# Optimization experiments

Measured on AMD Instinct MI355X. Metric: run time of the kernel, lower is better.

Reference implementation:

```python
import jax, jax.numpy as jnp
import numpy as np

MARGIN = 0.3
EPS = 1e-12


def setup_inputs() -> dict:
    key = jax.random.key(0)
    k1, k2 = jax.random.split(key)
    n, d = 4096, 1024
    inputs = jax.random.normal(k1, (n, d), dtype=jnp.float32)
    targets = jax.random.randint(k2, (n,), 0, 64, dtype=jnp.int64)
    return {"inputs": inputs, "targets": targets}


def reference(inputs, targets):
    n = inputs.shape[0]
    # pairwise Euclidean distance matrix: ||xi||^2 + ||xj||^2 - 2 xi.xj
    sq = jnp.sum(inputs * inputs, axis=1)  # [n]
    dist2 = sq[:, None] + sq[None, :] - 2.0 * (inputs @ inputs.T)
    dist = jnp.sqrt(jnp.clip(dist2, EPS))  # [n, n]
    # same-label mask (includes diagonal, matching original)
    mask = targets[:, None] == targets[None, :]
    # fused masked row-wise hard mining
    neg_inf = jnp.asarray(-jnp.inf, dist.dtype)
    pos_inf = jnp.asarray(jnp.inf, dist.dtype)
    dist_ap = jnp.max(jnp.where(mask, dist, neg_inf), axis=1)  # hardest positive
    dist_an = jnp.min(jnp.where(mask, pos_inf, dist), axis=1)  # hardest negative
    # MarginRankingLoss with y=1: mean(relu(margin - (dist_an - dist_ap)))
    loss = jnp.mean(jnp.maximum(MARGIN - (dist_an - dist_ap), 0.0))
    prec = jnp.sum((dist_an > dist_ap).astype(jnp.float32)) / n
    return (loss, prec)
```

## Files before the change

kernel.cpp:

```cpp
#include <hip/hip_runtime.h>
#include <stdint.h>

#define MARGIN 0.3f
#define EPS 1e-12f

typedef __attribute__((ext_vector_type(8))) __bf16 bf16x8;
typedef __attribute__((ext_vector_type(4))) float f32x4;

__device__ __forceinline__ unsigned short f2bf(float f) {
    unsigned u = __float_as_uint(f);
    unsigned r = (u + 0x7FFFu + ((u >> 16) & 1u)) >> 16;
    return (unsigned short)r;
}

#define GLD16(gp, lp)                                                     \
    __builtin_amdgcn_global_load_lds(                                     \
        (const __attribute__((address_space(1))) void*)(gp),              \
        (__attribute__((address_space(3))) void*)(lp), 16, 0, 0)

__global__ __launch_bounds__(256) void prep_kernel(
    const float* __restrict__ X, unsigned short* __restrict__ Xbf,
    float* __restrict__ sqg, unsigned* __restrict__ apb,
    unsigned* __restrict__ anb, int d) {
    const int row = blockIdx.x;
    const int tid = threadIdx.x;
    const float4* Xr = (const float4*)(X + (size_t)row * d);
    float s = 0.0f;
    for (int idx = tid; idx < (d >> 2); idx += blockDim.x) {
        float4 v = Xr[idx];
        s += v.x * v.x + v.y * v.y + v.z * v.z + v.w * v.w;
        ushort4 o;
        o.x = f2bf(v.x); o.y = f2bf(v.y); o.z = f2bf(v.z); o.w = f2bf(v.w);
        ((ushort4*)(Xbf + (size_t)row * d))[idx] = o;
    }
    __shared__ float red[4];
    for (int off = 32; off > 0; off >>= 1) s += __shfl_down(s, off, 64);
    const int wave = tid >> 6, lane = tid & 63;
    if (lane == 0) red[wave] = s;
    __syncthreads();
    if (tid == 0) {
        sqg[row] = red[0] + red[1] + red[2] + red[3];
        apb[row] = 0u;
        anb[row] = 0x7F800000u;
    }
}

#define BM 128
#define BN 128
#define BK 32

__global__ __launch_bounds__(256) void tri_gemm(
    const unsigned short* __restrict__ Xbf, const float* __restrict__ sqg,
    const int* __restrict__ tgt, unsigned* __restrict__ apb,
    unsigned* __restrict__ anb, int n, int d) {
    __shared__ unsigned short ldsA[BM * BK];
    __shared__ unsigned short ldsB[BN * BK];

    const int tid  = threadIdx.x;
    const int lane = tid & 63;
    const int wave = tid >> 6;
    const int wm = wave >> 1, wn = wave & 1;
    const int lo = lane & 15, hi = lane >> 4;
    const int rowBase = blockIdx.y * BM;
    const int colBase = blockIdx.x * BN;

    const int lrow = lane >> 2;
    const int lk   = (lane & 3) * 8;

    f32x4 acc[4][4] = {};

    for (int k0 = 0; k0 < d; k0 += BK) {
#pragma unroll
        for (int c2 = 0; c2 < 2; ++c2) {
            const int c = wave * 2 + c2;
            const unsigned short* gA =
                Xbf + (size_t)(rowBase + c * 16 + lrow) * d + k0 + lk;
            GLD16(gA, &ldsA[c * 512]);
            const unsigned short* gB =
                Xbf + (size_t)(colBase + c * 16 + lrow) * d + k0 + lk;
            GLD16(gB, &ldsB[c * 512]);
        }
        asm volatile("s_waitcnt vmcnt(0)" ::: "memory");
        __syncthreads();

        bf16x8 a[4], b[4];
#pragma unroll
        for (int mi = 0; mi < 4; ++mi)
            a[mi] = *(const bf16x8*)&ldsA[(wm * 64 + mi * 16 + lo) * BK + hi * 8];
#pragma unroll
        for (int ni = 0; ni < 4; ++ni)
            b[ni] = *(const bf16x8*)&ldsB[(wn * 64 + ni * 16 + lo) * BK + hi * 8];
#pragma unroll
        for (int mi = 0; mi < 4; ++mi)
#pragma unroll
            for (int ni = 0; ni < 4; ++ni)
                acc[mi][ni] = __builtin_amdgcn_mfma_f32_16x16x32_bf16(
                    a[mi], b[ni], acc[mi][ni], 0, 0, 0);
        __syncthreads();
    }

    float sqj[4];
    int   tj[4];
#pragma unroll
    for (int ni = 0; ni < 4; ++ni) {
        const int gj = colBase + wn * 64 + ni * 16 + lo;
        sqj[ni] = sqg[gj];
        tj[ni]  = tgt[gj];
    }
#pragma unroll
    for (int mi = 0; mi < 4; ++mi) {
#pragma unroll
        for (int j = 0; j < 4; ++j) {
            const int gi = rowBase + wm * 64 + mi * 16 + hi * 4 + j;
            const float sqi = sqg[gi];
            const int   ti  = tgt[gi];
            float ap = 0.0f;
            float an = __uint_as_float(0x7F800000u);
#pragma unroll
            for (int ni = 0; ni < 4; ++ni) {
                const float d2 = sqi + sqj[ni] - 2.0f * acc[mi][ni][j];
                const float dist = sqrtf(fmaxf(d2, EPS));
                if (ti == tj[ni]) ap = fmaxf(ap, dist);
                else              an = fminf(an, dist);
            }
#pragma unroll
            for (int m = 1; m < 16; m <<= 1) {
                ap = fmaxf(ap, __shfl_xor(ap, m, 64));
                an = fminf(an, __shfl_xor(an, m, 64));
            }
            if (lo == 0) {
                atomicMax(&apb[gi], __float_as_uint(ap));
                atomicMin(&anb[gi], __float_as_uint(an));
            }
        }
    }
}

__global__ __launch_bounds__(256) void finalize_kernel(
    const unsigned* __restrict__ apb, const unsigned* __restrict__ anb,
    float* __restrict__ out, int n) {
    const int tid = threadIdx.x;
    float ls = 0.0f, pc = 0.0f;
    for (int i = tid; i < n; i += blockDim.x) {
        const float ap = __uint_as_float(apb[i]);
        const float an = __uint_as_float(anb[i]);
        ls += fmaxf(MARGIN - (an - ap), 0.0f);
        pc += (an > ap) ? 1.0f : 0.0f;
    }
    __shared__ float rl[4], rp[4];
    for (int off = 32; off > 0; off >>= 1) {
        ls += __shfl_down(ls, off, 64);
        pc += __shfl_down(pc, off, 64);
    }
    const int wave = tid >> 6, lane = tid & 63;
    if (lane == 0) { rl[wave] = ls; rp[wave] = pc; }
    __syncthreads();
    if (tid == 0) {
        out[0] = (rl[0] + rl[1] + rl[2] + rl[3]) / (float)n;
        out[1] = (rp[0] + rp[1] + rp[2] + rp[3]) / (float)n;
    }
}

__global__ __launch_bounds__(256) void fb_zero(float* __restrict__ out) {
    if (threadIdx.x == 0) { out[0] = 0.0f; out[1] = 0.0f; }
}

__global__ __launch_bounds__(256) void fb_row(
    const float* __restrict__ X, const int* __restrict__ tgt,
    float* __restrict__ out, int n, int d) {
    __shared__ float xi[4096];
    const int i = blockIdx.x;
    const int tid = threadIdx.x;
    for (int k = tid; k < d; k += 256) xi[k] = X[(size_t)i * d + k];
    __syncthreads();
    const int ti = tgt[i];
    float ap = 0.0f;
    float an = __uint_as_float(0x7F800000u);
    for (int j = tid; j < n; j += 256) {
        const float4* Xj = (const float4*)(X + (size_t)j * d);
        float s = 0.0f;
        for (int k4 = 0; k4 < (d >> 2); ++k4) {
            float4 v = Xj[k4];
            float4 u = *(const float4*)&xi[k4 * 4];
            float dx = u.x - v.x, dy = u.y - v.y, dz = u.z - v.z, dw = u.w - v.w;
            s += dx * dx + dy * dy + dz * dz + dw * dw;
        }
        const float dist = sqrtf(fmaxf(s, EPS));
        if (tgt[j] == ti) ap = fmaxf(ap, dist);
        else              an = fminf(an, dist);
    }
    for (int m = 1; m < 64; m <<= 1) {
        ap = fmaxf(ap, __shfl_xor(ap, m, 64));
        an = fminf(an, __shfl_xor(an, m, 64));
    }
    __shared__ float rap[4], ran[4];
    const int wave = tid >> 6, lane = tid & 63;
    if (lane == 0) { rap[wave] = ap; ran[wave] = an; }
    __syncthreads();
    if (tid == 0) {
        ap = fmaxf(fmaxf(rap[0], rap[1]), fmaxf(rap[2], rap[3]));
        an = fminf(fminf(ran[0], ran[1]), fminf(ran[2], ran[3]));
        atomicAdd(&out[0], fmaxf(MARGIN - (an - ap), 0.0f));
        atomicAdd(&out[1], (an > ap) ? 1.0f : 0.0f);
    }
}

__global__ __launch_bounds__(64) void fb_scale(float* __restrict__ out, float inv_n) {
    if (threadIdx.x == 0) { out[0] *= inv_n; out[1] *= inv_n; }
}

extern "C" void kernel_launch(void* const* d_in, const int* in_sizes, int n_in,
                              void* d_out, int out_size, void* d_ws, size_t ws_size,
                              hipStream_t stream) {
    const float* X   = (const float*)d_in[0];
    const int*   tgt = (const int*)d_in[1];
    const int n = in_sizes[1];
    const int d = in_sizes[0] / n;

    const size_t need = (size_t)n * d * 2 + (size_t)n * 4 * 3;
    if (ws_size >= need) {
        char* ws = (char*)d_ws;
        unsigned short* Xbf = (unsigned short*)ws;
        float*    sqg = (float*)(ws + (size_t)n * d * 2);
        unsigned* apb = (unsigned*)((char*)sqg + (size_t)n * 4);
        unsigned* anb = apb + n;

        prep_kernel<<<n, 256, 0, stream>>>(X, Xbf, sqg, apb, anb, d);
        dim3 grid(n / BN, n / BM);
        tri_gemm<<<grid, 256, 0, stream>>>(Xbf, sqg, tgt, apb, anb, n, d);
        finalize_kernel<<<1, 256, 0, stream>>>(apb, anb, (float*)d_out, n);
    } else {
        fb_zero<<<1, 256, 0, stream>>>((float*)d_out);
        fb_row<<<n, 256, 0, stream>>>(X, tgt, (float*)d_out, n, d);
        fb_scale<<<1, 64, 0, stream>>>((float*)d_out, 1.0f / (float)n);
    }
}
```

Measured before the change: 145.8 us.

## Exploit distance symmetry with triangular tiles, double-buffer LDS, fuse finalize

Launches only lower-triangular 128x128 tiles of the symmetric distance matrix. Each off-diagonal tile also reduces along columns and updates the column rows' hardest positive and negative with atomics, which roughly halves the GEMM work. The K loop now double-buffers LDS so the next tile's global loads overlap the MFMAs. The separate finalize kernel is folded into the last finishing block through an atomic counter. The cost is extra column-reduction shuffles and atomics, plus a global-counter barrier pattern.

```diff
diff --git a/kernel.cpp b/kernel.cpp
--- a/kernel.cpp
+++ b/kernel.cpp
@@ -21,7 +21,7 @@
 __global__ __launch_bounds__(256) void prep_kernel(
     const float* __restrict__ X, unsigned short* __restrict__ Xbf,
     float* __restrict__ sqg, unsigned* __restrict__ apb,
-    unsigned* __restrict__ anb, int d) {
+    unsigned* __restrict__ anb, unsigned* __restrict__ ctr, int d) {
     const int row = blockIdx.x;
     const int tid = threadIdx.x;
     const float4* Xr = (const float4*)(X + (size_t)row * d);
@@ -42,6 +42,7 @@
         sqg[row] = red[0] + red[1] + red[2] + red[3];
         apb[row] = 0u;
         anb[row] = 0x7F800000u;
+        if (row == 0) ctr[0] = 0u;
     }
 }
 
@@ -52,51 +53,72 @@
 __global__ __launch_bounds__(256) void tri_gemm(
     const unsigned short* __restrict__ Xbf, const float* __restrict__ sqg,
     const int* __restrict__ tgt, unsigned* __restrict__ apb,
-    unsigned* __restrict__ anb, int n, int d) {
-    __shared__ unsigned short ldsA[BM * BK];
-    __shared__ unsigned short ldsB[BN * BK];
+    unsigned* __restrict__ anb, unsigned* __restrict__ ctr,
+    float* __restrict__ out, int n, int d, int nblk) {
+    __shared__ unsigned short ldsA[2][BM * BK];
+    __shared__ unsigned short ldsB[2][BN * BK];
 
     const int tid  = threadIdx.x;
     const int lane = tid & 63;
     const int wave = tid >> 6;
     const int wm = wave >> 1, wn = wave & 1;
     const int lo = lane & 15, hi = lane >> 4;
-    const int rowBase = blockIdx.y * BM;
-    const int colBase = blockIdx.x * BN;
+
+    const int bid = blockIdx.x;
+    int bi = (int)((sqrtf(8.0f * (float)bid + 1.0f) - 1.0f) * 0.5f);
+    while ((bi + 1) * (bi + 2) / 2 <= bid) ++bi;
+    while (bi * (bi + 1) / 2 > bid) --bi;
+    const int bj = bid - bi * (bi + 1) / 2;
+    const int rowBase = bi * BM;
+    const int colBase = bj * BN;
+    const bool offdiag = (bi != bj);
 
     const int lrow = lane >> 2;
     const int lk   = (lane & 3) * 8;
 
     f32x4 acc[4][4] = {};
 
-    for (int k0 = 0; k0 < d; k0 += BK) {
-#pragma unroll
-        for (int c2 = 0; c2 < 2; ++c2) {
-            const int c = wave * 2 + c2;
-            const unsigned short* gA =
-                Xbf + (size_t)(rowBase + c * 16 + lrow) * d + k0 + lk;
-            GLD16(gA, &ldsA[c * 512]);
-            const unsigned short* gB =
-                Xbf + (size_t)(colBase + c * 16 + lrow) * d + k0 + lk;
-            GLD16(gB, &ldsB[c * 512]);
-        }
-        asm volatile("s_waitcnt vmcnt(0)" ::: "memory");
-        __syncthreads();
-
+    const int nt = d / BK;
+    int cur = 0;
+#pragma unroll
+    for (int c2 = 0; c2 < 2; ++c2) {
+        const int c = wave * 2 + c2;
+        GLD16(Xbf + (size_t)(rowBase + c * 16 + lrow) * d + lk, &ldsA[0][c * 512]);
+        GLD16(Xbf + (size_t)(colBase + c * 16 + lrow) * d + lk, &ldsB[0][c * 512]);
+    }
+    asm volatile("s_waitcnt vmcnt(0)" ::: "memory");
+    __syncthreads();
+
+    for (int t = 0; t < nt; ++t) {
+        if (t + 1 < nt) {
+            const int k0 = (t + 1) * BK;
+#pragma unroll
+            for (int c2 = 0; c2 < 2; ++c2) {
+                const int c = wave * 2 + c2;
+                GLD16(Xbf + (size_t)(rowBase + c * 16 + lrow) * d + k0 + lk,
+                      &ldsA[cur ^ 1][c * 512]);
+                GLD16(Xbf + (size_t)(colBase + c * 16 + lrow) * d + k0 + lk,
+                      &ldsB[cur ^ 1][c * 512]);
+            }
+        }
         bf16x8 a[4], b[4];
 #pragma unroll
         for (int mi = 0; mi < 4; ++mi)
-            a[mi] = *(const bf16x8*)&ldsA[(wm * 64 + mi * 16 + lo) * BK + hi * 8];
+            a[mi] = *(const bf16x8*)&ldsA[cur][(wm * 64 + mi * 16 + lo) * BK + hi * 8];
 #pragma unroll
         for (int ni = 0; ni < 4; ++ni)
-            b[ni] = *(const bf16x8*)&ldsB[(wn * 64 + ni * 16 + lo) * BK + hi * 8];
+            b[ni] = *(const bf16x8*)&ldsB[cur][(wn * 64 + ni * 16 + lo) * BK + hi * 8];
 #pragma unroll
         for (int mi = 0; mi < 4; ++mi)
 #pragma unroll
             for (int ni = 0; ni < 4; ++ni)
                 acc[mi][ni] = __builtin_amdgcn_mfma_f32_16x16x32_bf16(
                     a[mi], b[ni], acc[mi][ni], 0, 0, 0);
-        __syncthreads();
+        if (t + 1 < nt) {
+            asm volatile("s_waitcnt vmcnt(0)" ::: "memory");
+            __syncthreads();
+            cur ^= 1;
+        }
     }
 
     float sqj[4];
@@ -107,6 +129,10 @@
         sqj[ni] = sqg[gj];
         tj[ni]  = tgt[gj];
     }
+    float cap[4], can[4];
+#pragma unroll
+    for (int ni = 0; ni < 4; ++ni) { cap[ni] = 0.0f; can[ni] = __uint_as_float(0x7F800000u); }
+
 #pragma unroll
     for (int mi = 0; mi < 4; ++mi) {
 #pragma unroll
@@ -120,8 +146,13 @@
             for (int ni = 0; ni < 4; ++ni) {
                 const float d2 = sqi + sqj[ni] - 2.0f * acc[mi][ni][j];
                 const float dist = sqrtf(fmaxf(d2, EPS));
-                if (ti == tj[ni]) ap = fmaxf(ap, dist);
-                else              an = fminf(an, dist);
+                if (ti == tj[ni]) {
+                    ap = fmaxf(ap, dist);
+                    cap[ni] = fmaxf(cap[ni], dist);
+                } else {
+                    an = fminf(an, dist);
+                    can[ni] = fminf(can[ni], dist);
+                }
             }
 #pragma unroll
             for (int m = 1; m < 16; m <<= 1) {
@@ -134,30 +165,53 @@
             }
         }
     }
-}
-
-__global__ __launch_bounds__(256) void finalize_kernel(
-    const unsigned* __restrict__ apb, const unsigned* __restrict__ anb,
-    float* __restrict__ out, int n) {
-    const int tid = threadIdx.x;
-    float ls = 0.0f, pc = 0.0f;
-    for (int i = tid; i < n; i += blockDim.x) {
-        const float ap = __uint_as_float(apb[i]);
-        const float an = __uint_as_float(anb[i]);
-        ls += fmaxf(MARGIN - (an - ap), 0.0f);
-        pc += (an > ap) ? 1.0f : 0.0f;
-    }
-    __shared__ float rl[4], rp[4];
-    for (int off = 32; off > 0; off >>= 1) {
-        ls += __shfl_down(ls, off, 64);
-        pc += __shfl_down(pc, off, 64);
-    }
-    const int wave = tid >> 6, lane = tid & 63;
-    if (lane == 0) { rl[wave] = ls; rp[wave] = pc; }
-    __syncthreads();
+    if (offdiag) {
+#pragma unroll
+        for (int ni = 0; ni < 4; ++ni) {
+            float ap = cap[ni], an = can[ni];
+#pragma unroll
+            for (int m = 16; m < 64; m <<= 1) {
+                ap = fmaxf(ap, __shfl_xor(ap, m, 64));
+                an = fminf(an, __shfl_xor(an, m, 64));
+            }
+            if (hi == 0) {
+                const int gj = colBase + wn * 64 + ni * 16 + lo;
+                atomicMax(&apb[gj], __float_as_uint(ap));
+                atomicMin(&anb[gj], __float_as_uint(an));
+            }
+        }
+    }
+
+    __threadfence();
+    __syncthreads();
+    __shared__ int lastFlag;
     if (tid == 0) {
-        out[0] = (rl[0] + rl[1] + rl[2] + rl[3]) / (float)n;
-        out[1] = (rp[0] + rp[1] + rp[2] + rp[3]) / (float)n;
+        unsigned prev = __hip_atomic_fetch_add(ctr, 1u, __ATOMIC_ACQ_REL,
+                                               __HIP_MEMORY_SCOPE_AGENT);
+        lastFlag = (prev == (unsigned)(nblk - 1)) ? 1 : 0;
+    }
+    __syncthreads();
+    if (lastFlag) {
+        float ls = 0.0f, pc = 0.0f;
+        for (int i = tid; i < n; i += 256) {
+            const float ap = __uint_as_float(__hip_atomic_load(
+                &apb[i], __ATOMIC_RELAXED, __HIP_MEMORY_SCOPE_AGENT));
+            const float an = __uint_as_float(__hip_atomic_load(
+                &anb[i], __ATOMIC_RELAXED, __HIP_MEMORY_SCOPE_AGENT));
+            ls += fmaxf(MARGIN - (an - ap), 0.0f);
+            pc += (an > ap) ? 1.0f : 0.0f;
+        }
+        __shared__ float rl[4], rp[4];
+        for (int off = 32; off > 0; off >>= 1) {
+            ls += __shfl_down(ls, off, 64);
+            pc += __shfl_down(pc, off, 64);
+        }
+        if ((tid & 63) == 0) { rl[tid >> 6] = ls; rp[tid >> 6] = pc; }
+        __syncthreads();
+        if (tid == 0) {
+            out[0] = (rl[0] + rl[1] + rl[2] + rl[3]) / (float)n;
+            out[1] = (rp[0] + rp[1] + rp[2] + rp[3]) / (float)n;
+        }
     }
 }
 
@@ -217,18 +271,20 @@
     const int n = in_sizes[1];
     const int d = in_sizes[0] / n;
 
-    const size_t need = (size_t)n * d * 2 + (size_t)n * 4 * 3;
+    const size_t need = (size_t)n * d * 2 + (size_t)n * 4 * 3 + 4;
     if (ws_size >= need) {
         char* ws = (char*)d_ws;
         unsigned short* Xbf = (unsigned short*)ws;
         float*    sqg = (float*)(ws + (size_t)n * d * 2);
         unsigned* apb = (unsigned*)((char*)sqg + (size_t)n * 4);
         unsigned* anb = apb + n;
-
-        prep_kernel<<<n, 256, 0, stream>>>(X, Xbf, sqg, apb, anb, d);
-        dim3 grid(n / BN, n / BM);
-        tri_gemm<<<grid, 256, 0, stream>>>(Xbf, sqg, tgt, apb, anb, n, d);
-        finalize_kernel<<<1, 256, 0, stream>>>(apb, anb, (float*)d_out, n);
+        unsigned* ctr = anb + n;
+
+        const int nb = n / BM;
+        const int nblk = nb * (nb + 1) / 2;
+        prep_kernel<<<n, 256, 0, stream>>>(X, Xbf, sqg, apb, anb, ctr, d);
+        tri_gemm<<<nblk, 256, 0, stream>>>(Xbf, sqg, tgt, apb, anb, ctr,
+                                           (float*)d_out, n, d, nblk);
     } else {
         fb_zero<<<1, 256, 0, stream>>>((float*)d_out);
         fb_row<<<n, 256, 0, stream>>>(X, tgt, (float*)d_out, n, d);
```

Measured after the change: 146.3 us. Within noise of the previous version (+0.3%).
